# Kernel optimization log

Hardware: AMD Instinct MI355X
Metric: run time of the kernel (lower is better)

Reference implementation:

```python
import jax, jax.numpy as jnp
import numpy as np

D_K = 64
D_MODEL = 1024
N_HEADS = 16


def setup_inputs() -> dict:
    key = jax.random.key(0)
    ks = jax.random.split(key, 9)
    B, S = 2, 2048
    scale = 1.0 / np.sqrt(D_MODEL)
    inp = {
        "x": jax.random.normal(ks[0], (B, S, D_MODEL), dtype=jnp.float32),
        "w_q": jax.random.normal(ks[1], (D_MODEL, N_HEADS * D_K), dtype=jnp.float32) * scale,
        "b_q": jnp.zeros((N_HEADS * D_K,), dtype=jnp.float32),
        "w_k": jax.random.normal(ks[2], (D_MODEL, N_HEADS * D_K), dtype=jnp.float32) * scale,
        "b_k": jnp.zeros((N_HEADS * D_K,), dtype=jnp.float32),
        "w_v": jax.random.normal(ks[3], (D_MODEL, N_HEADS * D_K), dtype=jnp.float32) * scale,
        "b_v": jnp.zeros((N_HEADS * D_K,), dtype=jnp.float32),
        "w_o": jax.random.normal(ks[4], (N_HEADS * D_K, D_MODEL), dtype=jnp.float32) * scale,
        "b_o": jnp.zeros((D_MODEL,), dtype=jnp.float32),
    }
    return inp


def reference(x, w_q, b_q, w_k, b_k, w_v, b_v, w_o, b_o):
    B, S, _ = x.shape
    H, Dk = N_HEADS, D_K

    def split_heads(m):  # [B,S,H*Dk] -> [B,H,S,Dk]
        return m.reshape(B, S, H, Dk).transpose(0, 2, 1, 3)

    Q = split_heads(x @ w_q + b_q)
    K = split_heads(x @ w_k + b_k)
    V = split_heads(x @ w_v + b_v)

    scores = jnp.einsum("bhsd,bhtd->bhst", Q, K) / jnp.sqrt(jnp.float32(Dk))
    probs = jax.nn.softmax(scores, axis=-1)
    attn = jnp.einsum("bhst,bhtd->bhsd", probs, V)  # [B,H,S,Dk]
    attn = attn.transpose(0, 2, 1, 3).reshape(B, S, H * Dk)
    return attn @ w_o + b_o
```

## Files before the change

### kernel.cpp

```cpp
#include <hip/hip_runtime.h>
#include <math.h>

#define D_MODELc 1024
#define N_HEADSc 16
#define D_Kc     64
#define B_SZc    2
#define S_LENc   2048
#define NTOKc    (B_SZc * S_LENc)

using half8  = __attribute__((ext_vector_type(8))) _Float16;
using half4  = __attribute__((ext_vector_type(4))) _Float16;
using fp16x2 = __attribute__((ext_vector_type(2))) __fp16;
using float4v = __attribute__((ext_vector_type(4))) float;

__global__ __launch_bounds__(256) void cvt_all(
    const float* __restrict__ x,
    const float* __restrict__ W0, const float* __restrict__ W1,
    const float* __restrict__ W2, const float* __restrict__ W3,
    _Float16* __restrict__ wout, _Float16* __restrict__ xout)
{
    __shared__ float T[32][33];
    const int z = blockIdx.z;
    const int t = threadIdx.x;

    if (z == 4) {
        const int bid = blockIdx.y * 32 + blockIdx.x;
        #pragma unroll
        for (int c = 0; c < 2; ++c) {
            const int i = bid * 512 + c * 256 + t;
            float4v a = ((const float4v*)x)[2 * i];
            float4v b = ((const float4v*)x)[2 * i + 1];
            half8 h;
            h[0] = (_Float16)a[0]; h[1] = (_Float16)a[1];
            h[2] = (_Float16)a[2]; h[3] = (_Float16)a[3];
            h[4] = (_Float16)b[0]; h[5] = (_Float16)b[1];
            h[6] = (_Float16)b[2]; h[7] = (_Float16)b[3];
            ((half8*)xout)[i] = h;
        }
        return;
    }

    const float* W = (z == 0) ? W0 : (z == 1) ? W1 : (z == 2) ? W2 : W3;
    _Float16* O = wout + (size_t)z * 1024 * 1024;

    const int k0 = blockIdx.x * 32;
    const int n0 = blockIdx.y * 32;
    {
        const int r = t >> 3, c4 = (t & 7) * 4;
        float4v v = *(const float4v*)(W + (size_t)(k0 + r) * 1024 + n0 + c4);
        T[r][c4 + 0] = v[0]; T[r][c4 + 1] = v[1];
        T[r][c4 + 2] = v[2]; T[r][c4 + 3] = v[3];
    }
    __syncthreads();
    {
        const int rn = t >> 3, ck4 = (t & 7) * 4;
        half4 h;
        h[0] = (_Float16)T[ck4 + 0][rn];
        h[1] = (_Float16)T[ck4 + 1][rn];
        h[2] = (_Float16)T[ck4 + 2][rn];
        h[3] = (_Float16)T[ck4 + 3][rn];
        *(half4*)(O + (size_t)(n0 + rn) * 1024 + k0 + ck4) = h;
    }
}

__global__ __launch_bounds__(256) void gemm_qkv(
    const _Float16* __restrict__ A, const _Float16* __restrict__ BtAll,
    const float* __restrict__ bias0, const float* __restrict__ bias1,
    const float* __restrict__ bias2, _Float16* __restrict__ Cout)
{
    __shared__ _Float16 Als[2][128 * 32];
    __shared__ _Float16 Bls[2][128 * 32];

    constexpr int K = 1024;
    const int tid = threadIdx.x;
    const int m0  = blockIdx.x * 128;
    const int n0  = blockIdx.y * 128;
    const int z   = blockIdx.z;

    const _Float16* Bt  = BtAll + (size_t)z * 1024 * 1024;
    const float* bias   = (z == 0) ? bias0 : (z == 1) ? bias1 : bias2;
    const float qscale  = (z == 0) ? 0.18033688011112042f : 1.0f;

    const int wave = tid >> 6, lane = tid & 63;
    const int wr = wave >> 1, wc = wave & 1;
    const int quad = lane >> 4, l16 = lane & 15;

    float4v acc[4][4];
    #pragma unroll
    for (int i = 0; i < 4; ++i)
        #pragma unroll
        for (int j = 0; j < 4; ++j)
            acc[i][j] = (float4v){0.f, 0.f, 0.f, 0.f};

    for (int k0 = 0; k0 < K; k0 += 64) {
        #pragma unroll
        for (int c = 0; c < 2; ++c) {
            const int i   = c * 256 + tid;
            const int row = i >> 2, kc = i & 3;
            #pragma unroll
            for (int h = 0; h < 2; ++h) {
                __builtin_amdgcn_global_load_lds(
                    (const __attribute__((address_space(1))) void*)
                        (A + (size_t)(m0 + row) * K + k0 + h * 32 + kc * 8),
                    (__attribute__((address_space(3))) void*)(Als[h] + i * 8),
                    16, 0, 0);
                __builtin_amdgcn_global_load_lds(
                    (const __attribute__((address_space(1))) void*)
                        (Bt + (size_t)(n0 + row) * K + k0 + h * 32 + kc * 8),
                    (__attribute__((address_space(3))) void*)(Bls[h] + i * 8),
                    16, 0, 0);
            }
        }
        __syncthreads();

        half8 af[4][2], bf[4][2];
        #pragma unroll
        for (int i = 0; i < 4; ++i) {
            const int r = (wr * 64 + i * 16 + l16) * 32 + quad * 8;
            af[i][0] = *(const half8*)(Als[0] + r);
            af[i][1] = *(const half8*)(Als[1] + r);
        }
        #pragma unroll
        for (int j = 0; j < 4; ++j) {
            const int r = (wc * 64 + j * 16 + l16) * 32 + quad * 8;
            bf[j][0] = *(const half8*)(Bls[0] + r);
            bf[j][1] = *(const half8*)(Bls[1] + r);
        }
        #pragma unroll
        for (int i = 0; i < 4; ++i)
            #pragma unroll
            for (int j = 0; j < 4; ++j) {
                acc[i][j] = __builtin_amdgcn_mfma_f32_16x16x32_f16(
                    af[i][0], bf[j][0], acc[i][j], 0, 0, 0);
                acc[i][j] = __builtin_amdgcn_mfma_f32_16x16x32_f16(
                    af[i][1], bf[j][1], acc[i][j], 0, 0, 0);
            }
        __syncthreads();
    }

    if (z != 2) {
        #pragma unroll
        for (int i = 0; i < 4; ++i) {
            const int rbase = m0 + wr * 64 + i * 16 + quad * 4;
            #pragma unroll
            for (int j = 0; j < 4; ++j) {
                const int col = n0 + wc * 64 + j * 16 + l16;
                const float bv = bias[col];
                #pragma unroll
                for (int r = 0; r < 4; ++r) {
                    const float v = (acc[i][j][r] + bv) * qscale;
                    const int n = rbase + r;
                    const int b = n >> 11, s = n & 2047;
                    const int h = col >> 6, d = col & 63;
                    _Float16* C = Cout + (size_t)z * NTOKc * D_MODELc;
                    C[(((size_t)(b * N_HEADSc + h)) * S_LENc + s) * D_Kc + d] =
                        (_Float16)v;
                }
            }
        }
    } else {
        #pragma unroll
        for (int i = 0; i < 4; ++i) {
            const int rbase = m0 + wr * 64 + i * 16 + quad * 4;
            const int b = rbase >> 11, s0 = rbase & 2047;
            #pragma unroll
            for (int j = 0; j < 4; ++j) {
                const int col = n0 + wc * 64 + j * 16 + l16;
                const float bv = bias[col];
                const int h = col >> 6, d = col & 63;
                half4 hv;
                #pragma unroll
                for (int r = 0; r < 4; ++r)
                    hv[r] = (_Float16)(acc[i][j][r] + bv);
                _Float16* C = Cout + (size_t)2 * NTOKc * D_MODELc;
                *(half4*)(C + (((size_t)(b * N_HEADSc + h)) * D_Kc + d) *
                          S_LENc + s0) = hv;
            }
        }
    }
}

__global__ __launch_bounds__(256) void gemm_out(
    const _Float16* __restrict__ A, const _Float16* __restrict__ Bt,
    const float* __restrict__ bias, float* __restrict__ C)
{
    __shared__ _Float16 Als[2][64 * 32];
    __shared__ _Float16 Bls[2][128 * 32];

    constexpr int K = 1024;
    const int tid = threadIdx.x;
    const int m0  = blockIdx.x * 64;
    const int n0  = blockIdx.y * 128;

    const int wave = tid >> 6, lane = tid & 63;
    const int wr = wave >> 1, wc = wave & 1;
    const int quad = lane >> 4, l16 = lane & 15;

    float4v acc[2][4];
    #pragma unroll
    for (int i = 0; i < 2; ++i)
        #pragma unroll
        for (int j = 0; j < 4; ++j)
            acc[i][j] = (float4v){0.f, 0.f, 0.f, 0.f};

    for (int k0 = 0; k0 < K; k0 += 64) {
        {
            const int row = tid >> 2, kc = tid & 3;
            #pragma unroll
            for (int h = 0; h < 2; ++h)
                __builtin_amdgcn_global_load_lds(
                    (const __attribute__((address_space(1))) void*)
                        (A + (size_t)(m0 + row) * K + k0 + h * 32 + kc * 8),
                    (__attribute__((address_space(3))) void*)(Als[h] + tid * 8),
                    16, 0, 0);
        }
        #pragma unroll
        for (int c = 0; c < 2; ++c) {
            const int i = c * 256 + tid;
            const int row = i >> 2, kc = i & 3;
            #pragma unroll
            for (int h = 0; h < 2; ++h)
                __builtin_amdgcn_global_load_lds(
                    (const __attribute__((address_space(1))) void*)
                        (Bt + (size_t)(n0 + row) * K + k0 + h * 32 + kc * 8),
                    (__attribute__((address_space(3))) void*)(Bls[h] + i * 8),
                    16, 0, 0);
        }
        __syncthreads();

        half8 af[2][2], bf[4][2];
        #pragma unroll
        for (int i = 0; i < 2; ++i) {
            const int r = (wr * 32 + i * 16 + l16) * 32 + quad * 8;
            af[i][0] = *(const half8*)(Als[0] + r);
            af[i][1] = *(const half8*)(Als[1] + r);
        }
        #pragma unroll
        for (int j = 0; j < 4; ++j) {
            const int r = (wc * 64 + j * 16 + l16) * 32 + quad * 8;
            bf[j][0] = *(const half8*)(Bls[0] + r);
            bf[j][1] = *(const half8*)(Bls[1] + r);
        }
        #pragma unroll
        for (int i = 0; i < 2; ++i)
            #pragma unroll
            for (int j = 0; j < 4; ++j) {
                acc[i][j] = __builtin_amdgcn_mfma_f32_16x16x32_f16(
                    af[i][0], bf[j][0], acc[i][j], 0, 0, 0);
                acc[i][j] = __builtin_amdgcn_mfma_f32_16x16x32_f16(
                    af[i][1], bf[j][1], acc[i][j], 0, 0, 0);
            }
        __syncthreads();
    }

    #pragma unroll
    for (int i = 0; i < 2; ++i) {
        const int rbase = m0 + wr * 32 + i * 16 + quad * 4;
        #pragma unroll
        for (int j = 0; j < 4; ++j) {
            const int col = n0 + wc * 64 + j * 16 + l16;
            const float bv = bias[col];
            #pragma unroll
            for (int r = 0; r < 4; ++r)
                C[(size_t)(rbase + r) * 1024 + col] = acc[i][j][r] + bv;
        }
    }
}

__global__ __launch_bounds__(256) void attn_mfma(
    const _Float16* __restrict__ Qb, const _Float16* __restrict__ Kb,
    const _Float16* __restrict__ Vtg, _Float16* __restrict__ Op,
    float* __restrict__ Lp)
{
    constexpr int PS = 72;
    __shared__ _Float16 Ks[64 * PS];
    __shared__ _Float16 Vt[64 * PS];
    __shared__ _Float16 Ps[128 * PS];

    const int tid  = threadIdx.x;
    const int wv   = tid >> 6;
    const int lane = tid & 63;
    const int quad = lane >> 4;
    const int l16  = lane & 15;

    const int q0 = blockIdx.x * 128;
    const int bh = blockIdx.y;
    const int sp = blockIdx.z;
    const int kb = sp * (S_LENc / 2);
    const int kend = kb + S_LENc / 2;

    const _Float16* Qsl = Qb  + (size_t)bh * S_LENc * D_Kc;
    const _Float16* Ksl = Kb  + (size_t)bh * S_LENc * D_Kc;
    const _Float16* Vsl = Vtg + (size_t)bh * S_LENc * D_Kc;

    half8 aq[2][2];
    #pragma unroll
    for (int qf = 0; qf < 2; ++qf) {
        const int row = q0 + wv * 32 + qf * 16 + l16;
        aq[qf][0] = *(const half8*)(Qsl + (size_t)row * 64 + quad * 8);
        aq[qf][1] = *(const half8*)(Qsl + (size_t)row * 64 + 32 + quad * 8);
    }

    float4v O[2][4];
    #pragma unroll
    for (int qf = 0; qf < 2; ++qf)
        #pragma unroll
        for (int nt = 0; nt < 4; ++nt)
            O[qf][nt] = (float4v){0.f, 0.f, 0.f, 0.f};
    float lr[2] = {0.f, 0.f};

    const int sr = tid >> 2;
    const int sg = (tid & 3) * 16;

    for (int t0 = kb; t0 < kend; t0 += 64) {
        half8 k0 = *(const half8*)(Ksl + (size_t)(t0 + sr) * 64 + sg);
        half8 k1 = *(const half8*)(Ksl + (size_t)(t0 + sr) * 64 + sg + 8);
        half8 v0 = *(const half8*)(Vsl + (size_t)sr * S_LENc + t0 + sg);
        half8 v1 = *(const half8*)(Vsl + (size_t)sr * S_LENc + t0 + sg + 8);
        __syncthreads();
        *(half8*)(Ks + sr * PS + sg)     = k0;
        *(half8*)(Ks + sr * PS + sg + 8) = k1;
        *(half8*)(Vt + sr * PS + sg)     = v0;
        *(half8*)(Vt + sr * PS + sg + 8) = v1;
        __syncthreads();

        half8 kf[4][2];
        #pragma unroll
        for (int nt = 0; nt < 4; ++nt) {
            kf[nt][0] = *(const half8*)(Ks + (nt * 16 + l16) * PS + quad * 8);
            kf[nt][1] = *(const half8*)(Ks + (nt * 16 + l16) * PS + 32 + quad * 8);
        }

        #pragma unroll
        for (int qf = 0; qf < 2; ++qf) {
            float4v st[4];
            #pragma unroll
            for (int nt = 0; nt < 4; ++nt) {
                st[nt] = __builtin_amdgcn_mfma_f32_16x16x32_f16(
                    kf[nt][0], aq[qf][0], (float4v){0.f, 0.f, 0.f, 0.f}, 0, 0, 0);
                st[nt] = __builtin_amdgcn_mfma_f32_16x16x32_f16(
                    kf[nt][1], aq[qf][1], st[nt], 0, 0, 0);
            }
            float ls = 0.f;
            #pragma unroll
            for (int nt = 0; nt < 4; ++nt) {
                const float p0 = __builtin_amdgcn_exp2f(fminf(st[nt][0], 15.5f));
                const float p1 = __builtin_amdgcn_exp2f(fminf(st[nt][1], 15.5f));
                const float p2 = __builtin_amdgcn_exp2f(fminf(st[nt][2], 15.5f));
                const float p3 = __builtin_amdgcn_exp2f(fminf(st[nt][3], 15.5f));
                ls += (p0 + p1) + (p2 + p3);
                union { fp16x2 h2[2]; half4 h4; } u;
                u.h2[0] = __builtin_amdgcn_cvt_pkrtz(p0, p1);
                u.h2[1] = __builtin_amdgcn_cvt_pkrtz(p2, p3);
                *(half4*)(Ps + (wv * 32 + qf * 16 + l16) * PS +
                          nt * 16 + quad * 4) = u.h4;
            }
            lr[qf] += ls;
        }

        half8 bvv[4][2];
        #pragma unroll
        for (int nt = 0; nt < 4; ++nt) {
            bvv[nt][0] = *(const half8*)(Vt + (nt * 16 + l16) * PS + quad * 8);
            bvv[nt][1] = *(const half8*)(Vt + (nt * 16 + l16) * PS + 32 + quad * 8);
        }
        #pragma unroll
        for (int qf = 0; qf < 2; ++qf) {
            half8 ap0 = *(const half8*)(Ps + (wv * 32 + qf * 16 + l16) * PS + quad * 8);
            half8 ap1 = *(const half8*)(Ps + (wv * 32 + qf * 16 + l16) * PS + 32 + quad * 8);
            #pragma unroll
            for (int nt = 0; nt < 4; ++nt) {
                O[qf][nt] = __builtin_amdgcn_mfma_f32_16x16x32_f16(
                    ap0, bvv[nt][0], O[qf][nt], 0, 0, 0);
                O[qf][nt] = __builtin_amdgcn_mfma_f32_16x16x32_f16(
                    ap1, bvv[nt][1], O[qf][nt], 0, 0, 0);
            }
        }
    }

    const size_t qgb = (size_t)bh * S_LENc;
    #pragma unroll
    for (int qf = 0; qf < 2; ++qf) {
        float t = lr[qf];
        t += __shfl_xor(t, 16, 64);
        t += __shfl_xor(t, 32, 64);
        if (quad == 0)
            Lp[(size_t)sp * 65536 + qgb + q0 + wv * 32 + qf * 16 + l16] = t;
        #pragma unroll
        for (int r = 0; r < 4; ++r) {
            const int q = q0 + wv * 32 + qf * 16 + quad * 4 + r;
            _Float16* dst = Op + ((size_t)sp * 65536 + qgb + q) * 64;
            #pragma unroll
            for (int nt = 0; nt < 4; ++nt)
                dst[nt * 16 + l16] = (_Float16)O[qf][nt][r];
        }
    }
}

__global__ __launch_bounds__(256) void attn_combine(
    const _Float16* __restrict__ Op, const float* __restrict__ Lp,
    _Float16* __restrict__ Ab)
{
    const int i  = blockIdx.x * 256 + threadIdx.x;
    const int e0 = i * 8;
    const int qg = e0 >> 6;
    const int d0 = e0 & 63;
    const int bh = qg >> 11, q = qg & 2047;
    const int b  = bh >> 4,  h = bh & 15;

    const float inv = 1.0f / (Lp[qg] + Lp[65536 + qg]);
    half8 o0 = *(const half8*)(Op + (size_t)qg * 64 + d0);
    half8 o1 = *(const half8*)(Op + ((size_t)65536 + qg) * 64 + d0);
    half8 hv;
    #pragma unroll
    for (int j = 0; j < 8; ++j)
        hv[j] = (_Float16)(((float)o0[j] + (float)o1[j]) * inv);
    *(half8*)(Ab + ((size_t)(b * S_LENc + q)) * 1024 + h * 64 + d0) = hv;
}

extern "C" void kernel_launch(void* const* d_in, const int* in_sizes, int n_in,
                              void* d_out, int out_size, void* d_ws, size_t ws_size,
                              hipStream_t stream)
{
    const float* x  = (const float*)d_in[0];
    const float* wq = (const float*)d_in[1];
    const float* bq = (const float*)d_in[2];
    const float* wk = (const float*)d_in[3];
    const float* bk = (const float*)d_in[4];
    const float* wv = (const float*)d_in[5];
    const float* bv = (const float*)d_in[6];
    const float* wo = (const float*)d_in[7];
    const float* bo = (const float*)d_in[8];
    float* out = (float*)d_out;

    const size_t M1 = 1024 * 1024;
    const size_t M4 = 4 * M1;
    _Float16* xh = (_Float16*)d_ws;
    _Float16* wh = xh + M4;
    _Float16* Qh = wh + M4;
    _Float16* Oph = Qh + 3 * M4;
    float*    Lp  = (float*)(Oph + 2 * M4);
    _Float16* Ah = xh;

    cvt_all<<<dim3(32, 32, 5), dim3(256), 0, stream>>>(
        x, wq, wk, wv, wo, wh, xh);
    gemm_qkv<<<dim3(NTOKc / 128, D_MODELc / 128, 3), dim3(256), 0, stream>>>(
        xh, wh, bq, bk, bv, Qh);
    attn_mfma<<<dim3(S_LENc / 128, B_SZc * N_HEADSc, 2), dim3(256), 0, stream>>>(
        Qh, Qh + M4, Qh + 2 * M4, Oph, Lp);
    attn_combine<<<dim3(NTOKc * D_MODELc / 8 / 256), dim3(256), 0, stream>>>(
        Oph, Lp, Ah);
    gemm_out<<<dim3(NTOKc / 64, D_MODELc / 128), dim3(256), 0, stream>>>(
        Ah, wh + 3 * M1, bo, out);
}
```

Before: 208.2 us.

## Prefetch next K/V tile into registers, XOR-swizzle LDS, and raise MFMA priority

The attention kernel now loads the next K/V tile from global memory into registers while the current tile is being computed, so load latency overlaps with MFMA and exp work. The padded LDS layouts (row stride 72) are replaced by unpadded 64-wide rows with an XOR swizzle on the 8-element groups, which reduces bank conflicts and LDS footprint. s_setprio is raised around the MFMA blocks to favour matrix issue across waves. The prefetch adds register pressure, which could lower occupancy.

```diff
diff --git a/kernel.cpp b/kernel.cpp
--- a/kernel.cpp
+++ b/kernel.cpp
@@ -272,16 +272,16 @@
     const _Float16* __restrict__ Vtg, _Float16* __restrict__ Op,
     float* __restrict__ Lp)
 {
-    constexpr int PS = 72;
-    __shared__ _Float16 Ks[64 * PS];
-    __shared__ _Float16 Vt[64 * PS];
-    __shared__ _Float16 Ps[128 * PS];
+    __shared__ _Float16 Ks[64 * 64];
+    __shared__ _Float16 Vt[64 * 64];
+    __shared__ _Float16 Ps[128 * 64];
 
     const int tid  = threadIdx.x;
     const int wv   = tid >> 6;
     const int lane = tid & 63;
     const int quad = lane >> 4;
     const int l16  = lane & 15;
+    const int sw   = (l16 & 7) << 3;
 
     const int q0 = blockIdx.x * 128;
     const int bh = blockIdx.y;
@@ -309,31 +309,45 @@
             O[qf][nt] = (float4v){0.f, 0.f, 0.f, 0.f};
     float lr[2] = {0.f, 0.f};
 
-    const int sr = tid >> 2;
-    const int sg = (tid & 3) * 16;
+    const int sr  = tid >> 2;
+    const int sg  = (tid & 3) * 16;
+    const int swS = (sr & 7) << 3;
+    const int wA  = (sr * 64 + sg) ^ swS;
+    const int wB  = (sr * 64 + sg + 8) ^ swS;
+
+    half8 k0 = *(const half8*)(Ksl + (size_t)(kb + sr) * 64 + sg);
+    half8 k1 = *(const half8*)(Ksl + (size_t)(kb + sr) * 64 + sg + 8);
+    half8 v0 = *(const half8*)(Vsl + (size_t)sr * S_LENc + kb + sg);
+    half8 v1 = *(const half8*)(Vsl + (size_t)sr * S_LENc + kb + sg + 8);
 
     for (int t0 = kb; t0 < kend; t0 += 64) {
-        half8 k0 = *(const half8*)(Ksl + (size_t)(t0 + sr) * 64 + sg);
-        half8 k1 = *(const half8*)(Ksl + (size_t)(t0 + sr) * 64 + sg + 8);
-        half8 v0 = *(const half8*)(Vsl + (size_t)sr * S_LENc + t0 + sg);
-        half8 v1 = *(const half8*)(Vsl + (size_t)sr * S_LENc + t0 + sg + 8);
-        __syncthreads();
-        *(half8*)(Ks + sr * PS + sg)     = k0;
-        *(half8*)(Ks + sr * PS + sg + 8) = k1;
-        *(half8*)(Vt + sr * PS + sg)     = v0;
-        *(half8*)(Vt + sr * PS + sg + 8) = v1;
-        __syncthreads();
+        __syncthreads();
+        *(half8*)(Ks + wA) = k0;
+        *(half8*)(Ks + wB) = k1;
+        *(half8*)(Vt + wA) = v0;
+        *(half8*)(Vt + wB) = v1;
+        __syncthreads();
+
+        const int tn = t0 + 64;
+        if (tn < kend) {
+            k0 = *(const half8*)(Ksl + (size_t)(tn + sr) * 64 + sg);
+            k1 = *(const half8*)(Ksl + (size_t)(tn + sr) * 64 + sg + 8);
+            v0 = *(const half8*)(Vsl + (size_t)sr * S_LENc + tn + sg);
+            v1 = *(const half8*)(Vsl + (size_t)sr * S_LENc + tn + sg + 8);
+        }
 
         half8 kf[4][2];
         #pragma unroll
         for (int nt = 0; nt < 4; ++nt) {
-            kf[nt][0] = *(const half8*)(Ks + (nt * 16 + l16) * PS + quad * 8);
-            kf[nt][1] = *(const half8*)(Ks + (nt * 16 + l16) * PS + 32 + quad * 8);
+            const int base = (nt * 16 + l16) * 64;
+            kf[nt][0] = *(const half8*)(Ks + ((base + quad * 8) ^ sw));
+            kf[nt][1] = *(const half8*)(Ks + ((base + 32 + quad * 8) ^ sw));
         }
 
         #pragma unroll
         for (int qf = 0; qf < 2; ++qf) {
             float4v st[4];
+            __builtin_amdgcn_s_setprio(1);
             #pragma unroll
             for (int nt = 0; nt < 4; ++nt) {
                 st[nt] = __builtin_amdgcn_mfma_f32_16x16x32_f16(
@@ -341,7 +355,9 @@
                 st[nt] = __builtin_amdgcn_mfma_f32_16x16x32_f16(
                     kf[nt][1], aq[qf][1], st[nt], 0, 0, 0);
             }
+            __builtin_amdgcn_s_setprio(0);
             float ls = 0.f;
+            const int rowP = (wv * 32 + qf * 16 + l16) * 64;
             #pragma unroll
             for (int nt = 0; nt < 4; ++nt) {
                 const float p0 = __builtin_amdgcn_exp2f(fminf(st[nt][0], 15.5f));
@@ -352,8 +368,7 @@
                 union { fp16x2 h2[2]; half4 h4; } u;
                 u.h2[0] = __builtin_amdgcn_cvt_pkrtz(p0, p1);
                 u.h2[1] = __builtin_amdgcn_cvt_pkrtz(p2, p3);
-                *(half4*)(Ps + (wv * 32 + qf * 16 + l16) * PS +
-                          nt * 16 + quad * 4) = u.h4;
+                *(half4*)(Ps + ((rowP + nt * 16 + quad * 4) ^ sw)) = u.h4;
             }
             lr[qf] += ls;
         }
@@ -361,13 +376,16 @@
         half8 bvv[4][2];
         #pragma unroll
         for (int nt = 0; nt < 4; ++nt) {
-            bvv[nt][0] = *(const half8*)(Vt + (nt * 16 + l16) * PS + quad * 8);
-            bvv[nt][1] = *(const half8*)(Vt + (nt * 16 + l16) * PS + 32 + quad * 8);
+            const int base = (nt * 16 + l16) * 64;
+            bvv[nt][0] = *(const half8*)(Vt + ((base + quad * 8) ^ sw));
+            bvv[nt][1] = *(const half8*)(Vt + ((base + 32 + quad * 8) ^ sw));
         }
         #pragma unroll
         for (int qf = 0; qf < 2; ++qf) {
-            half8 ap0 = *(const half8*)(Ps + (wv * 32 + qf * 16 + l16) * PS + quad * 8);
-            half8 ap1 = *(const half8*)(Ps + (wv * 32 + qf * 16 + l16) * PS + 32 + quad * 8);
+            const int rowP = (wv * 32 + qf * 16 + l16) * 64;
+            half8 ap0 = *(const half8*)(Ps + ((rowP + quad * 8) ^ sw));
+            half8 ap1 = *(const half8*)(Ps + ((rowP + 32 + quad * 8) ^ sw));
+            __builtin_amdgcn_s_setprio(1);
             #pragma unroll
             for (int nt = 0; nt < 4; ++nt) {
                 O[qf][nt] = __builtin_amdgcn_mfma_f32_16x16x32_f16(
@@ -375,6 +393,7 @@
                 O[qf][nt] = __builtin_amdgcn_mfma_f32_16x16x32_f16(
                     ap1, bvv[nt][1], O[qf][nt], 0, 0, 0);
             }
+            __builtin_amdgcn_s_setprio(0);
         }
     }
 
```

Result: no change. 208.2 us (-0.0%).

## Load K/V fragments directly from global memory, drop LDS staging and barriers

Applied to the files above, without the earlier changes.

The attention kernel no longer stages K and V tiles through shared memory with two block barriers per iteration. Each wave now reads its MFMA K and V fragments straight from global memory, relying on L1/L2 for reuse across the four waves, and launch bounds request four blocks per CU to raise occupancy. This removes the barrier stalls and LDS traffic and frees LDS, at the cost of four times more global/L1 load traffic for K and V and no explicit prefetch overlap.

```diff
diff --git a/kernel.cpp b/kernel.cpp
--- a/kernel.cpp
+++ b/kernel.cpp
@@ -267,14 +267,12 @@
     }
 }
 
-__global__ __launch_bounds__(256) void attn_mfma(
+__global__ __launch_bounds__(256, 4) void attn_mfma(
     const _Float16* __restrict__ Qb, const _Float16* __restrict__ Kb,
     const _Float16* __restrict__ Vtg, _Float16* __restrict__ Op,
     float* __restrict__ Lp)
 {
     constexpr int PS = 72;
-    __shared__ _Float16 Ks[64 * PS];
-    __shared__ _Float16 Vt[64 * PS];
     __shared__ _Float16 Ps[128 * PS];
 
     const int tid  = threadIdx.x;
@@ -309,26 +307,14 @@
             O[qf][nt] = (float4v){0.f, 0.f, 0.f, 0.f};
     float lr[2] = {0.f, 0.f};
 
-    const int sr = tid >> 2;
-    const int sg = (tid & 3) * 16;
-
     for (int t0 = kb; t0 < kend; t0 += 64) {
-        half8 k0 = *(const half8*)(Ksl + (size_t)(t0 + sr) * 64 + sg);
-        half8 k1 = *(const half8*)(Ksl + (size_t)(t0 + sr) * 64 + sg + 8);
-        half8 v0 = *(const half8*)(Vsl + (size_t)sr * S_LENc + t0 + sg);
-        half8 v1 = *(const half8*)(Vsl + (size_t)sr * S_LENc + t0 + sg + 8);
-        __syncthreads();
-        *(half8*)(Ks + sr * PS + sg)     = k0;
-        *(half8*)(Ks + sr * PS + sg + 8) = k1;
-        *(half8*)(Vt + sr * PS + sg)     = v0;
-        *(half8*)(Vt + sr * PS + sg + 8) = v1;
-        __syncthreads();
-
         half8 kf[4][2];
         #pragma unroll
         for (int nt = 0; nt < 4; ++nt) {
-            kf[nt][0] = *(const half8*)(Ks + (nt * 16 + l16) * PS + quad * 8);
-            kf[nt][1] = *(const half8*)(Ks + (nt * 16 + l16) * PS + 32 + quad * 8);
+            const _Float16* kp =
+                Ksl + (size_t)(t0 + nt * 16 + l16) * 64 + quad * 8;
+            kf[nt][0] = *(const half8*)(kp);
+            kf[nt][1] = *(const half8*)(kp + 32);
         }
 
         #pragma unroll
@@ -342,6 +328,7 @@
                     kf[nt][1], aq[qf][1], st[nt], 0, 0, 0);
             }
             float ls = 0.f;
+            const int rowP = (wv * 32 + qf * 16 + l16) * PS;
             #pragma unroll
             for (int nt = 0; nt < 4; ++nt) {
                 const float p0 = __builtin_amdgcn_exp2f(fminf(st[nt][0], 15.5f));
@@ -352,8 +339,7 @@
                 union { fp16x2 h2[2]; half4 h4; } u;
                 u.h2[0] = __builtin_amdgcn_cvt_pkrtz(p0, p1);
                 u.h2[1] = __builtin_amdgcn_cvt_pkrtz(p2, p3);
-                *(half4*)(Ps + (wv * 32 + qf * 16 + l16) * PS +
-                          nt * 16 + quad * 4) = u.h4;
+                *(half4*)(Ps + rowP + nt * 16 + quad * 4) = u.h4;
             }
             lr[qf] += ls;
         }
@@ -361,13 +347,16 @@
         half8 bvv[4][2];
         #pragma unroll
         for (int nt = 0; nt < 4; ++nt) {
-            bvv[nt][0] = *(const half8*)(Vt + (nt * 16 + l16) * PS + quad * 8);
-            bvv[nt][1] = *(const half8*)(Vt + (nt * 16 + l16) * PS + 32 + quad * 8);
+            const _Float16* vp =
+                Vsl + (size_t)(nt * 16 + l16) * S_LENc + t0 + quad * 8;
+            bvv[nt][0] = *(const half8*)(vp);
+            bvv[nt][1] = *(const half8*)(vp + 32);
         }
         #pragma unroll
         for (int qf = 0; qf < 2; ++qf) {
-            half8 ap0 = *(const half8*)(Ps + (wv * 32 + qf * 16 + l16) * PS + quad * 8);
-            half8 ap1 = *(const half8*)(Ps + (wv * 32 + qf * 16 + l16) * PS + 32 + quad * 8);
+            const int rowP = (wv * 32 + qf * 16 + l16) * PS;
+            half8 ap0 = *(const half8*)(Ps + rowP + quad * 8);
+            half8 ap1 = *(const half8*)(Ps + rowP + 32 + quad * 8);
             #pragma unroll
             for (int nt = 0; nt < 4; ++nt) {
                 O[qf][nt] = __builtin_amdgcn_mfma_f32_16x16x32_f16(
```

New measurement: 272.0 us. +30.7%, slower.
